# Performance work log

Measured on AMD Instinct MI355X. Metric: run time of the kernel, lower is better.

Reference implementation:

```python
import jax, jax.numpy as jnp
import numpy as np

B, T, D = 16, 512, 256          # batch, seq_len, d_model (= num features = num graph nodes N)
H, MC, K, DE, DH = 4, 4, 3, 10, 128
GS, SS, AS = 4, 6, 4            # global/sector/asset regime states
TAU = 0.5
STEPS = 3                       # diffusion steps
HID = max(64, D)
DEC_H = max(64, D // 2)


def setup_inputs() -> dict:
    key = jax.random.key(0)
    ks = iter(jax.random.split(key, 64))

    def nrm(shape, s=0.02):
        return (s * jax.random.normal(next(ks), shape)).astype(jnp.float32)

    z = lambda *s: jnp.zeros(s, jnp.float32)
    o = lambda *s: jnp.ones(s, jnp.float32)
    p = dict(
        x=jax.random.normal(next(ks), (B, T, D), dtype=jnp.float32),
        # hierarchical regime controller
        gW1=nrm((D, HID)), gb1=z(HID), g_ln_w=o(HID), g_ln_b=z(HID),
        gW2=nrm((HID, GS)), gb2=z(GS),
        sW1=nrm((D, HID)), sb1=z(HID), sW2=nrm((HID, D * SS)), sb2=z(D * SS),
        aW1=nrm((D, HID)), ab1=z(HID), aW2=nrm((HID, D * AS)), ab2=z(D * AS),
        global_prior=z(GS), sector_prior=z(SS), asset_prior=z(AS),
        g2f=nrm((GS, D)),
        sector_emb=jax.random.normal(next(ks), (SS, D), dtype=jnp.float32),
        asset_emb=jax.random.normal(next(ks), (AS, D), dtype=jnp.float32),
        # bidirectional temporal scan (BI-Mamba stand-in)
        decay_f=nrm((D,), 1.0), decay_b=nrm((D,), 1.0),
        tW=nrm((D, D)), tb=z(D),
        # Bayesian MAGAC + diffusion graph prior
        psi=nrm((H, D, DE), 0.1), log_sigma=jnp.full((H,), -2.0, jnp.float32),
        step_logits=jnp.linspace(-1.0, 0.5, STEPS).astype(jnp.float32),
        noise_scale=jnp.full((STEPS,), 0.05, jnp.float32),
        Wk=nrm((K + 1, T, DH)),
        mean_w=nrm((DH,)), mean_b=z(), lv_w=nrm((DH,)), lv_b=z(),
        # risk-aware decoder
        dW1=nrm((D, DEC_H)), db1=z(DEC_H), d_ln_w=o(DEC_H), d_ln_b=z(DEC_H),
        mW=nrm((DEC_H,)), mb=z(), lvW=nrm((DEC_H,)), lvb=z(),
        cW=nrm((DEC_H,)), cb=z(),
    )
    return p


def _ln(h, w, b):
    m = h.mean(-1, keepdims=True)
    v = h.var(-1, keepdims=True)  # biased, matches torch LayerNorm
    return (h - m) / jnp.sqrt(v + 1e-5) * w + b


def _gelu(h):
    return jax.nn.gelu(h, approximate=False)


def _gumbel_softmax(k, logits):
    u = jax.random.uniform(k, logits.shape, minval=1e-6, maxval=1.0 - 1e-6)
    g = -jnp.log(-jnp.log(u))
    return jax.nn.softmax((logits + g) / TAU, axis=-1)


def _fwd(x, gW1, gb1, g_ln_w, g_ln_b, gW2, gb2, sW1, sb1, sW2, sb2,
         aW1, ab1, aW2, ab2, global_prior, sector_prior, asset_prior,
         g2f, sector_emb, asset_emb, decay_f, decay_b, tW, tb,
         psi, log_sigma, step_logits, noise_scale, Wk,
         mean_w, mean_b, lv_w, lv_b,
         dW1, db1, d_ln_w, d_ln_b, mW, mb, lvW, lvb, cW, cb):
    rk = jax.random.key(42)
    k_g, k_s, k_a, k_eps, k_diff = jax.random.split(rk, 5)

    # ---- hierarchical regime controller ----
    seq_mean = x.mean(1)                               # (B, D)
    diff_summary = (x[:, 1:] - x[:, :-1]).mean(1)      # (B, D)
    g_logits = _gelu(_ln(seq_mean @ gW1 + gb1, g_ln_w, g_ln_b)) @ gW2 + gb2
    s_logits = (_gelu(seq_mean @ sW1 + sb1) @ sW2 + sb2).reshape(B, D, SS)
    a_logits = (_gelu(diff_summary @ aW1 + ab1) @ aW2 + ab2).reshape(B, D, AS)
    g_probs = _gumbel_softmax(k_g, g_logits)
    s_probs = _gumbel_softmax(k_s, s_logits)
    a_probs = _gumbel_softmax(k_a, a_logits)
    global_gate = g_probs @ g2f                                   # (B, D)
    # diagonal of einsum('bfs,sd->bfd') == einsum('bfs,sf->bf')
    sector_gate = jnp.einsum('bfs,sf->bf', s_probs, sector_emb)
    asset_gate = jnp.einsum('bfs,sf->bf', a_probs, asset_emb)
    feature_gate = jax.nn.sigmoid(global_gate + sector_gate + asset_gate)
    gated_x = x * feature_gate[:, None, :]

    # ---- bidirectional temporal EMA scan (BI-Mamba stand-in) ----
    af = jax.nn.sigmoid(decay_f)
    abk = jax.nn.sigmoid(decay_b)
    xs = gated_x.transpose(1, 0, 2)                    # (T, B, D)

    def ema(a):
        def step(h, xt):
            h = a * h + (1.0 - a) * xt
            return h, h
        return step

    _, hf = jax.lax.scan(ema(af), jnp.zeros_like(xs[0]), xs)
    _, hb = jax.lax.scan(ema(abk), jnp.zeros_like(xs[0]), xs[::-1])
    temporal = (hf + hb[::-1]).transpose(1, 0, 2) @ tW + tb       # (B, T, D)
    node_major = temporal.transpose(0, 2, 1)                      # (B, N=D, T)

    # ---- Bayesian adjacency sampling (MC samples per head) ----
    logits = jnp.einsum('hne,hme->hnm', psi, psi) / jnp.sqrt(jnp.float32(DE))
    sigma = jnp.exp(log_sigma)                                    # (H,)
    eps = jax.random.normal(k_eps, (MC, H, D, D))
    A = jax.nn.softmax(logits[None] + sigma[None, :, None, None] * eps, axis=-1)

    # ---- diffusion refinement guided by regime features ----
    ctx = feature_gate.mean(0)
    ctx = ctx / (jnp.linalg.norm(ctx) + 1e-6)
    outer = ctx[:, None] * ctx[None, :]
    outer = outer / jnp.maximum(outer.sum(-1, keepdims=True), 1e-6)
    dkeys = jax.random.split(k_diff, STEPS)
    for s in range(STEPS):                             # fixed small loop, vectorized over (MC,H)
        alpha = jax.nn.sigmoid(step_logits[s])
        noise = noise_scale[s] * jax.random.normal(dkeys[s], A.shape)
        A = alpha * A + (1.0 - alpha) * outer + noise
        A = 0.5 * (A + jnp.swapaxes(A, -1, -2))
        A = jax.nn.softmax(A, axis=-1)

    # ---- K-hop graph conv, averaged over MC samples and heads ----
    Z = jnp.einsum('bnt,td->bnd', node_major, Wk[0])[None, None]  # hop 0
    P = jnp.broadcast_to(node_major, (MC, H, B, D, T))
    for k in range(1, K + 1):
        P = jnp.einsum('mhnp,mhbpt->mhbnt', A, P)
        Z = Z + jnp.einsum('mhbnt,td->mhbnd', P, Wk[k])
    Z = Z.mean((0, 1))                                            # (B, N, DH)
    graph_mean = Z @ mean_w + mean_b                              # (B, N)
    graph_logvar = Z @ lv_w + lv_b                                # (B, N)

    # ---- risk-aware decoder ----
    feat = _ln(_gelu(graph_mean @ dW1 + db1), d_ln_w, d_ln_b)     # (B, DEC_H)
    mean = feat @ mW + mb
    dec_logvar = feat @ lvW + lvb
    _cvar = jax.nn.sigmoid(feat @ cW + cb)  # auxiliary head (not in returned output)
    var = jnp.exp(dec_logvar) + jnp.exp(graph_logvar).sum(1)
    log_var = jnp.log(var)
    return jnp.stack([mean, log_var], axis=-1)                    # (B, 2)


def reference(x, gW1, gb1, g_ln_w, g_ln_b, gW2, gb2, sW1, sb1, sW2, sb2,
              aW1, ab1, aW2, ab2, global_prior, sector_prior, asset_prior,
              g2f, sector_emb, asset_emb, decay_f, decay_b, tW, tb,
              psi, log_sigma, step_logits, noise_scale, Wk,
              mean_w, mean_b, lv_w, lv_b,
              dW1, db1, d_ln_w, d_ln_b, mW, mb, lvW, lvb, cW, cb):
    return _fwd(x, gW1, gb1, g_ln_w, g_ln_b, gW2, gb2, sW1, sb1, sW2, sb2,
                aW1, ab1, aW2, ab2, global_prior, sector_prior, asset_prior,
                g2f, sector_emb, asset_emb, decay_f, decay_b, tW, tb,
                psi, log_sigma, step_logits, noise_scale, Wk,
                mean_w, mean_b, lv_w, lv_b,
                dW1, db1, d_ln_w, d_ln_b, mW, mb, lvW, lvb, cW, cb)
```

## Files before the change

### kernel.cpp

```cpp
#include <hip/hip_runtime.h>
#include <stdint.h>

#define PARTITIONABLE 1

namespace {

struct TFPair { uint32_t a, b; };

__host__ __device__ constexpr uint32_t rotl32(uint32_t x, int d) {
  return (x << d) | (x >> (32 - d));
}

__host__ __device__ constexpr TFPair tf2x32(uint32_t k0, uint32_t k1,
                                            uint32_t x0, uint32_t x1) {
  uint32_t k2 = k0 ^ k1 ^ 0x1BD11BDAu;
  x0 += k0; x1 += k1;
  x0 += x1; x1 = rotl32(x1, 13); x1 ^= x0;
  x0 += x1; x1 = rotl32(x1, 15); x1 ^= x0;
  x0 += x1; x1 = rotl32(x1, 26); x1 ^= x0;
  x0 += x1; x1 = rotl32(x1, 6);  x1 ^= x0;
  x0 += k1; x1 += k2 + 1u;
  x0 += x1; x1 = rotl32(x1, 17); x1 ^= x0;
  x0 += x1; x1 = rotl32(x1, 29); x1 ^= x0;
  x0 += x1; x1 = rotl32(x1, 16); x1 ^= x0;
  x0 += x1; x1 = rotl32(x1, 24); x1 ^= x0;
  x0 += k2; x1 += k0 + 2u;
  x0 += x1; x1 = rotl32(x1, 13); x1 ^= x0;
  x0 += x1; x1 = rotl32(x1, 15); x1 ^= x0;
  x0 += x1; x1 = rotl32(x1, 26); x1 ^= x0;
  x0 += x1; x1 = rotl32(x1, 6);  x1 ^= x0;
  x0 += k0; x1 += k1 + 3u;
  x0 += x1; x1 = rotl32(x1, 17); x1 ^= x0;
  x0 += x1; x1 = rotl32(x1, 29); x1 ^= x0;
  x0 += x1; x1 = rotl32(x1, 16); x1 ^= x0;
  x0 += x1; x1 = rotl32(x1, 24); x1 ^= x0;
  x0 += k1; x1 += k2 + 4u;
  x0 += x1; x1 = rotl32(x1, 13); x1 ^= x0;
  x0 += x1; x1 = rotl32(x1, 15); x1 ^= x0;
  x0 += x1; x1 = rotl32(x1, 26); x1 ^= x0;
  x0 += x1; x1 = rotl32(x1, 6);  x1 ^= x0;
  x0 += k2; x1 += k0 + 5u;
  return TFPair{x0, x1};
}

#if PARTITIONABLE
constexpr TFPair KG  = tf2x32(0u, 42u, 0u, 0u);
constexpr TFPair KS  = tf2x32(0u, 42u, 0u, 1u);
constexpr TFPair KA  = tf2x32(0u, 42u, 0u, 2u);
constexpr TFPair KE  = tf2x32(0u, 42u, 0u, 3u);
constexpr TFPair KD  = tf2x32(0u, 42u, 0u, 4u);
constexpr TFPair DK0 = tf2x32(KD.a, KD.b, 0u, 0u);
constexpr TFPair DK1 = tf2x32(KD.a, KD.b, 0u, 1u);
constexpr TFPair DK2 = tf2x32(KD.a, KD.b, 0u, 2u);
#else
constexpr TFPair SP0 = tf2x32(0u, 42u, 0u, 5u);
constexpr TFPair SP1 = tf2x32(0u, 42u, 1u, 6u);
constexpr TFPair SP2 = tf2x32(0u, 42u, 2u, 7u);
constexpr TFPair SP3 = tf2x32(0u, 42u, 3u, 8u);
constexpr TFPair SP4 = tf2x32(0u, 42u, 4u, 9u);
constexpr TFPair KG  = TFPair{SP0.a, SP1.a};
constexpr TFPair KS  = TFPair{SP2.a, SP3.a};
constexpr TFPair KA  = TFPair{SP4.a, SP0.b};
constexpr TFPair KE  = TFPair{SP1.b, SP2.b};
constexpr TFPair KD  = TFPair{SP3.b, SP4.b};
constexpr TFPair DP0 = tf2x32(KD.a, KD.b, 0u, 3u);
constexpr TFPair DP1 = tf2x32(KD.a, KD.b, 1u, 4u);
constexpr TFPair DP2 = tf2x32(KD.a, KD.b, 2u, 5u);
constexpr TFPair DK0 = TFPair{DP0.a, DP1.a};
constexpr TFPair DK1 = TFPair{DP2.a, DP0.b};
constexpr TFPair DK2 = TFPair{DP1.b, DP2.b};
#endif

__device__ __forceinline__ uint32_t rbits(uint32_t k0, uint32_t k1,
                                          uint32_t idx, uint32_t half) {
#if PARTITIONABLE
  TFPair t = tf2x32(k0, k1, 0u, idx);
  return t.a ^ t.b;
#else
  if (idx < half) return tf2x32(k0, k1, idx, idx + half).a;
  return tf2x32(k0, k1, idx - half, idx).b;
#endif
}

__device__ __forceinline__ float bits_to_u01(uint32_t bits) {
  return __uint_as_float((bits >> 9) | 0x3F800000u) - 1.0f;
}

__device__ __forceinline__ float gumbel_u(uint32_t k0, uint32_t k1,
                                          uint32_t idx, uint32_t half) {
  const float mn = 1e-6f;
  const float mx = 1.0f - 1e-6f;
  float f = bits_to_u01(rbits(k0, k1, idx, half));
  return fmaxf(mn, f * (mx - mn) + mn);
}

__device__ __forceinline__ float erfinv_f32(float x) {
  float w = -log1pf(-x * x);
  float p;
  if (w < 5.0f) {
    w -= 2.5f;
    p = 2.81022636e-08f;
    p = fmaf(p, w, 3.43273939e-07f);
    p = fmaf(p, w, -3.5233877e-06f);
    p = fmaf(p, w, -4.39150654e-06f);
    p = fmaf(p, w, 0.00021858087f);
    p = fmaf(p, w, -0.00125372503f);
    p = fmaf(p, w, -0.00417768164f);
    p = fmaf(p, w, 0.246640727f);
    p = fmaf(p, w, 1.50140941f);
  } else {
    w = sqrtf(w) - 3.0f;
    p = -0.000200214257f;
    p = fmaf(p, w, 0.000100950558f);
    p = fmaf(p, w, 0.00134934322f);
    p = fmaf(p, w, -0.00367342844f);
    p = fmaf(p, w, 0.00573950773f);
    p = fmaf(p, w, -0.0076224613f);
    p = fmaf(p, w, 0.00943887047f);
    p = fmaf(p, w, 1.00167406f);
    p = fmaf(p, w, 2.83297682f);
  }
  return p * x;
}

__device__ __forceinline__ float normal_from(uint32_t k0, uint32_t k1,
                                             uint32_t idx, uint32_t half) {
  const float lo = -0x1.fffffep-1f;
  float f = bits_to_u01(rbits(k0, k1, idx, half));
  float u = fmaxf(lo, f * 2.0f + lo);
  return 1.41421356237f * erfinv_f32(u);
}

__device__ __forceinline__ float gelu_f(float x) {
  return 0.5f * x * (1.0f + erff(x / 1.4142135623730951f));
}
__device__ __forceinline__ float sigmoid_f(float x) {
  return 1.0f / (1.0f + expf(-x));
}

__device__ __forceinline__ float wave_sum(float v) {
  #pragma unroll
  for (int m = 32; m > 0; m >>= 1) v += __shfl_xor(v, m);
  return v;
}
__device__ __forceinline__ float wave_max(float v) {
  #pragma unroll
  for (int m = 32; m > 0; m >>= 1) v = fmaxf(v, __shfl_xor(v, m));
  return v;
}
template <int NW>
__device__ __forceinline__ float blk_sum(float v, float* slots) {
  v = wave_sum(v);
  int wid = threadIdx.x >> 6;
  if ((threadIdx.x & 63) == 0) slots[wid] = v;
  __syncthreads();
  float r = slots[0];
  #pragma unroll
  for (int i = 1; i < NW; ++i) r += slots[i];
  return r;
}
template <int NW>
__device__ __forceinline__ float blk_max(float v, float* slots) {
  v = wave_max(v);
  int wid = threadIdx.x >> 6;
  if ((threadIdx.x & 63) == 0) slots[wid] = v;
  __syncthreads();
  float r = slots[0];
  #pragma unroll
  for (int i = 1; i < NW; ++i) r = fmaxf(r, slots[i]);
  return r;
}

struct Params {
  const float *x, *gW1, *gb1, *glnw, *glnb, *gW2, *gb2, *sW1, *sb1, *sW2, *sb2,
      *aW1, *ab1, *aW2, *ab2, *g2f, *semb, *aemb, *decay_f, *decay_b, *tW, *tb,
      *psi, *log_sigma, *step_logits, *noise_scale, *Wk, *mean_w, *mean_b,
      *lv_w, *lv_b, *dW1, *db1, *dlnw, *dlnb, *mW, *mb, *lvW, *lvb;
  float* out;
  float *ps, *ds, *hgG, *hgS, *hgA, *fg, *ctx, *v, *sv, *u, *Pf, *Qf, *Pb, *Qb,
      *Lf, *Lb, *YH, *R1, *R2, *gm, *glv, *A, *A2;
};


__device__ __forceinline__ void phase_hidden(const Params& P, float* smem,
                                             int bid, int tid) {
  float* inv = smem;
  float* s1 = smem + 256;
  float* s2 = smem + 260;
  int head = bid >> 4, b = bid & 15;
  float iv;
  if (head < 2) {
    float s = 0.f;
    for (int tc = 0; tc < 16; ++tc) s += P.ps[(size_t)(b * 16 + tc) * 256 + tid];
    iv = s / 512.0f;
  } else {
    iv = P.ds[b * 256 + tid];
  }
  inv[tid] = iv;
  __syncthreads();
  const float* W1 = (head == 0) ? P.gW1 : (head == 1) ? P.sW1 : P.aW1;
  const float* b1 = (head == 0) ? P.gb1 : (head == 1) ? P.sb1 : P.ab1;
  float h = b1[tid];
  for (int d = 0; d < 256; ++d) h = fmaf(inv[d], W1[d * 256 + tid], h);
  if (head == 0) {
    float mean = blk_sum<4>(h, s1) / 256.0f;
    float dv = h - mean;
    float var = blk_sum<4>(dv * dv, s2) / 256.0f;
    h = dv / sqrtf(var + 1e-5f) * P.glnw[tid] + P.glnb[tid];
  }
  float* outp = (head == 0) ? P.hgG : (head == 1) ? P.hgS : P.hgA;
  outp[b * 256 + tid] = gelu_f(h);
}

__device__ __forceinline__ void phase_vcompute(const Params& P, int bid2,
                                               int tid) {
  int j = bid2 >> 2, tg = bid2 & 3;
  const float* wp = (j & 1) ? P.lv_w : P.mean_w;
  const float* Wkk = P.Wk + (size_t)(j >> 1) * 65536;
  int wid = tid >> 6, lane = tid & 63;
  float w0 = wp[lane], w1 = wp[64 + lane];
  float svloc = 0.f;
  for (int i = 0; i < 32; ++i) {
    int t = tg * 128 + wid * 32 + i;
    const float* row = Wkk + (size_t)t * 128;
    float s = row[lane] * w0 + row[64 + lane] * w1;
    s = wave_sum(s);
    if (lane == 0) { P.v[j * 512 + t] = s; svloc += s; }
  }
  if (lane == 0) atomicAdd(&P.sv[j], svloc);
}

__device__ __forceinline__ void phase_ainit_row(const Params& P, float* smem,
                                                int blk, int tid) {
  float* pn = smem;
  float* s1 = smem + 12;
  float* s2 = smem + 16;
  int mh = blk >> 8, h = mh & 3, n = blk & 255, p = tid;
  if (p < 10) pn[p] = P.psi[(size_t)(h * 256 + n) * 10 + p];
  __syncthreads();
  const float* pp = P.psi + (size_t)(h * 256 + p) * 10;
  float s = 0.f;
  #pragma unroll
  for (int e = 0; e < 10; ++e) s = fmaf(pn[e], pp[e], s);
  float logit = s / sqrtf(10.0f);
  uint32_t idx = (uint32_t)blk * 256u + (uint32_t)p;
  float eps = normal_from(KE.a, KE.b, idx, 524288u);
  float val = logit + expf(P.log_sigma[h]) * eps;
  float mx = blk_max<4>(val, s1);
  float e = expf(val - mx);
  float sum = blk_sum<4>(e, s2);
  P.A[(size_t)blk * 256 + p] = e / sum;
}

__device__ __forceinline__ void phase_gates(const Params& P, float* smem,
                                            int bid, int tid) {
  float* hgGs = smem;
  float* hgSs = smem + 256;
  float* hgAs = smem + 512;
  float* lvS = smem + 768;
  float* lvA = smem + 1152;
  float* gsl = smem + 1408;
  float* gvals = smem + 1424;
  float* gpv = smem + 1428;
  int b = bid >> 2, f0 = (bid & 3) * 64;
  hgGs[tid] = P.hgG[b * 256 + tid];
  hgSs[tid] = P.hgS[b * 256 + tid];
  hgAs[tid] = P.hgA[b * 256 + tid];
  __syncthreads();
  float lg[4];
  #pragma unroll
  for (int s = 0; s < 4; ++s)
    lg[s] = blk_sum<4>(hgGs[tid] * P.gW2[tid * 4 + s], gsl + 4 * s);
  if (tid < 4) {
    float u = gumbel_u(KG.a, KG.b, (uint32_t)(b * 4 + tid), 32u);
    float g = -logf(-logf(u));
    gvals[tid] = (lg[tid] + P.gb2[tid] + g) / 0.5f;
  }
  __syncthreads();
  if (tid < 4) {
    float mx = fmaxf(fmaxf(gvals[0], gvals[1]), fmaxf(gvals[2], gvals[3]));
    float sum = expf(gvals[0] - mx) + expf(gvals[1] - mx) +
                expf(gvals[2] - mx) + expf(gvals[3] - mx);
    gpv[tid] = expf(gvals[tid] - mx) / sum;
  }
  {
    int o = tid;
    int fl = o / 6, s = o - fl * 6;
    int f = f0 + fl;
    const float* wp = P.sW2 + f * 6 + s;
    float acc = P.sb2[f * 6 + s];
    for (int d = 0; d < 256; ++d) acc = fmaf(hgSs[d], wp[(size_t)d * 1536], acc);
    float u = gumbel_u(KS.a, KS.b, (uint32_t)(b * 256 + f) * 6u + s, 12288u);
    lvS[o] = (acc + (-logf(-logf(u)))) / 0.5f;
  }
  if (tid < 128) {
    int o = tid + 256;
    int fl = o / 6, s = o - fl * 6;
    int f = f0 + fl;
    const float* wp = P.sW2 + f * 6 + s;
    float acc = P.sb2[f * 6 + s];
    for (int d = 0; d < 256; ++d) acc = fmaf(hgSs[d], wp[(size_t)d * 1536], acc);
    float u = gumbel_u(KS.a, KS.b, (uint32_t)(b * 256 + f) * 6u + s, 12288u);
    lvS[o] = (acc + (-logf(-logf(u)))) / 0.5f;
  }
  {
    int fl = tid >> 2, s = tid & 3;
    int f = f0 + fl;
    const float* wp = P.aW2 + f * 4 + s;
    float acc = P.ab2[f * 4 + s];
    for (int d = 0; d < 256; ++d) acc = fmaf(hgAs[d], wp[(size_t)d * 1024], acc);
    float u = gumbel_u(KA.a, KA.b, (uint32_t)(b * 256 + f) * 4u + s, 8192u);
    lvA[tid] = (acc + (-logf(-logf(u)))) / 0.5f;
  }
  __syncthreads();
  if (tid < 64) {
    int f = f0 + tid;
    float v0 = lvS[tid * 6 + 0], v1 = lvS[tid * 6 + 1], v2 = lvS[tid * 6 + 2];
    float v3 = lvS[tid * 6 + 3], v4 = lvS[tid * 6 + 4], v5 = lvS[tid * 6 + 5];
    float mx = fmaxf(fmaxf(fmaxf(v0, v1), fmaxf(v2, v3)), fmaxf(v4, v5));
    float e0 = expf(v0 - mx), e1 = expf(v1 - mx), e2 = expf(v2 - mx);
    float e3 = expf(v3 - mx), e4 = expf(v4 - mx), e5 = expf(v5 - mx);
    float ssum = e0 + e1 + e2 + e3 + e4 + e5;
    float sg = (e0 / ssum) * P.semb[0 * 256 + f] + (e1 / ssum) * P.semb[1 * 256 + f] +
               (e2 / ssum) * P.semb[2 * 256 + f] + (e3 / ssum) * P.semb[3 * 256 + f] +
               (e4 / ssum) * P.semb[4 * 256 + f] + (e5 / ssum) * P.semb[5 * 256 + f];
    float a0 = lvA[tid * 4 + 0], a1 = lvA[tid * 4 + 1];
    float a2 = lvA[tid * 4 + 2], a3 = lvA[tid * 4 + 3];
    float amx = fmaxf(fmaxf(a0, a1), fmaxf(a2, a3));
    float x0 = expf(a0 - amx), x1 = expf(a1 - amx);
    float x2 = expf(a2 - amx), x3 = expf(a3 - amx);
    float asum = x0 + x1 + x2 + x3;
    float ag = (x0 / asum) * P.aemb[0 * 256 + f] + (x1 / asum) * P.aemb[1 * 256 + f] +
               (x2 / asum) * P.aemb[2 * 256 + f] + (x3 / asum) * P.aemb[3 * 256 + f];
    float gg = 0.f;
    #pragma unroll
    for (int s = 0; s < 4; ++s) gg = fmaf(gpv[s], P.g2f[s * 256 + f], gg);
    P.fg[b * 256 + f] = sigmoid_f(gg + sg + ag);
  }
}

__device__ __forceinline__ void phase_ctx(const Params& P, float* smem,
                                          int tid) {
  float* s1 = smem;
  float* s2 = smem + 4;
  float c = 0.f;
  for (int b = 0; b < 16; ++b) c += P.fg[b * 256 + tid];
  c /= 16.0f;
  float ss = blk_sum<4>(c * c, s1);
  float cv = c / (sqrtf(ss) + 1e-6f);
  P.ctx[tid] = cv;
  float S = blk_sum<4>(cv, s2);
  if (tid == 0) P.ctx[256] = S;
}

__device__ __forceinline__ void phase_scan1(const Params& P, float* smem,
                                            int ch, int tid) {
  float* vv = smem;
  int b = ch >> 4, c = ch & 15;
  int d = tid;
  vv[(d >> 5) * 32 + (d & 31)] = P.v[(d >> 5) * 512 + c * 32 + (d & 31)];
  __syncthreads();
  float g = P.fg[b * 256 + d];
  float af = sigmoid_f(P.decay_f[d]);
  float ab = sigmoid_f(P.decay_b[d]);
  float r_gx[32];
  const float* xp = P.x + ((size_t)b * 512 + c * 32) * 256 + d;
  #pragma unroll
  for (int i = 0; i < 32; ++i) r_gx[i] = xp[(size_t)i * 256] * g;
  float h = 0.f, pw = 1.f;
  float Pr[8], Q[8];
  #pragma unroll
  for (int j = 0; j < 8; ++j) { Pr[j] = 0.f; Q[j] = 0.f; }
  #pragma unroll
  for (int i = 0; i < 32; ++i) {
    h = fmaf(af, h, (1.0f - af) * r_gx[i]);
    pw *= af;
    #pragma unroll
    for (int j = 0; j < 8; ++j) {
      float vj = vv[j * 32 + i];
      Pr[j] = fmaf(h, vj, Pr[j]);
      Q[j] = fmaf(pw, vj, Q[j]);
    }
  }
  size_t base = ((size_t)(b * 16 + c) * 8) * 256 + d;
  #pragma unroll
  for (int j = 0; j < 8; ++j) {
    P.Pf[base + j * 256] = Pr[j];
    P.Qf[base + j * 256] = Q[j];
  }
  P.Lf[(b * 16 + c) * 256 + d] = h;
  h = 0.f; pw = 1.f;
  #pragma unroll
  for (int j = 0; j < 8; ++j) { Pr[j] = 0.f; Q[j] = 0.f; }
  #pragma unroll
  for (int i = 31; i >= 0; --i) {
    h = fmaf(ab, h, (1.0f - ab) * r_gx[i]);
    pw *= ab;
    #pragma unroll
    for (int j = 0; j < 8; ++j) {
      float vj = vv[j * 32 + i];
      Pr[j] = fmaf(h, vj, Pr[j]);
      Q[j] = fmaf(pw, vj, Q[j]);
    }
  }
  #pragma unroll
  for (int j = 0; j < 8; ++j) {
    P.Pb[base + j * 256] = Pr[j];
    P.Qb[base + j * 256] = Q[j];
  }
  P.Lb[(b * 16 + c) * 256 + d] = h;
}

__device__ __forceinline__ void phase_scan2(const Params& P, int blk, int tid) {
  int b = blk >> 3, j = blk & 7;
  int d = tid;
  float af = sigmoid_f(P.decay_f[d]);
  float ab = sigmoid_f(P.decay_b[d]);
  float af32 = af, ab32 = ab;
  #pragma unroll
  for (int q = 0; q < 5; ++q) { af32 *= af32; ab32 *= ab32; }
  float acc = 0.f, H = 0.f;
  for (int c = 0; c < 16; ++c) {
    size_t base = ((size_t)(b * 16 + c) * 8 + j) * 256 + d;
    acc += P.Pf[base] + H * P.Qf[base];
    H = P.Lf[(b * 16 + c) * 256 + d] + af32 * H;
  }
  H = 0.f;
  for (int c = 15; c >= 0; --c) {
    size_t base = ((size_t)(b * 16 + c) * 8 + j) * 256 + d;
    acc += P.Pb[base] + H * P.Qb[base];
    H = P.Lb[(b * 16 + c) * 256 + d] + ab32 * H;
  }
  P.u[(b * 8 + j) * 256 + d] = acc;
}

__device__ __forceinline__ void phase_ygemm(const Params& P, float* smem,
                                            int blk32, int tid) {
  float* As = smem;
  float* Bs = smem + 1056;
  float* svs = smem + 2112;
  int n0 = (blk32 & 7) * 32, m0 = (blk32 >> 3) * 32;
  int tx = tid & 31, ty = tid >> 5;
  if (tid < 8) svs[tid] = P.sv[tid];
  float acc[4] = {0.f, 0.f, 0.f, 0.f};
  for (int k0 = 0; k0 < 256; k0 += 32) {
    #pragma unroll
    for (int l = 0; l < 4; ++l) {
      int e = tid + l * 256, r = e >> 5, cc = e & 31;
      As[r * 33 + cc] = P.u[(size_t)(m0 + r) * 256 + k0 + cc];
      Bs[r * 33 + cc] = P.tW[(size_t)(k0 + r) * 256 + n0 + cc];
    }
    __syncthreads();
    #pragma unroll
    for (int kk = 0; kk < 32; ++kk) {
      float bv = Bs[kk * 33 + tx];
      #pragma unroll
      for (int i = 0; i < 4; ++i)
        acc[i] = fmaf(As[(ty + 8 * i) * 33 + kk], bv, acc[i]);
    }
    __syncthreads();
  }
  int n = n0 + tx;
  float tbn = P.tb[n];
  float mb0 = P.mean_b[0], lb0 = P.lv_b[0];
  #pragma unroll
  for (int i = 0; i < 4; ++i) {
    int row = m0 + ty + 8 * i;
    int b = row >> 3, j = row & 7;
    float val = acc[i] + tbn * svs[j];
    if (j == 0) P.gm[b * 256 + n] = val + mb0;
    else if (j == 1) P.glv[b * 256 + n] = val + lb0;
    else {
      int k = (j >> 1) - 1, proj = j & 1;
      P.YH[k * 8192 + n * 32 + b * 2 + proj] = val;
    }
  }
}

__device__ __forceinline__ void phase_mix_row(const Params& P, float* smem,
                                              int sidx, const float* Ain,
                                              float* Aout, uint32_t dk0,
                                              uint32_t dk1, int blk, int tid) {
  float* s1 = smem;
  float* s2 = smem + 4;
  float alpha = sigmoid_f(P.step_logits[sidx]);
  float ns = P.noise_scale[sidx];
  float S = P.ctx[256];
  float cp = P.ctx[tid];
  int mh = blk >> 8, n = blk & 255, p = tid;
  float cn = P.ctx[n];
  float o_np = (cn * cp) / fmaxf(cn * S, 1e-6f);
  float o_pn = (cp * cn) / fmaxf(cp * S, 1e-6f);
  uint32_t i_np = (uint32_t)blk * 256u + (uint32_t)p;
  uint32_t i_pn = (uint32_t)mh * 65536u + (uint32_t)p * 256u + (uint32_t)n;
  float a_np = Ain[(size_t)mh * 65536 + n * 256 + p];
  float a_pn = Ain[(size_t)mh * 65536 + p * 256 + n];
  float m_np = alpha * a_np + (1.0f - alpha) * o_np +
               ns * normal_from(dk0, dk1, i_np, 524288u);
  float m_pn = alpha * a_pn + (1.0f - alpha) * o_pn +
               ns * normal_from(dk0, dk1, i_pn, 524288u);
  float val = 0.5f * (m_np + m_pn);
  float mx = blk_max<4>(val, s1);
  float e = expf(val - mx);
  float sum = blk_sum<4>(e, s2);
  Aout[(size_t)blk * 256 + p] = e / sum;
}

__device__ __forceinline__ void phase_horner(const Params& P, float* smem,
                                             const float* A, const float* Rin,
                                             int sRin, const float* Yadd,
                                             float* Rout, int bid, int tid) {
  float* As = smem;
  float* Bs = smem + 1056;
  int nt = bid & 7, mh = bid >> 3;
  int n0 = nt * 32;
  int tx = tid & 31, ty = tid >> 5;
  float acc[4] = {0.f, 0.f, 0.f, 0.f};
  const float* Ab = A + (size_t)mh * 65536;
  const float* Rb = Rin + (size_t)mh * sRin;
  for (int k0 = 0; k0 < 256; k0 += 32) {
    #pragma unroll
    for (int l = 0; l < 4; ++l) {
      int e = tid + l * 256, r = e >> 5, cc = e & 31;
      As[r * 33 + cc] = Ab[(size_t)(n0 + r) * 256 + k0 + cc];
      Bs[r * 33 + cc] = Rb[(size_t)(k0 + r) * 32 + cc];
    }
    __syncthreads();
    #pragma unroll
    for (int kk = 0; kk < 32; ++kk) {
      float bv = Bs[kk * 33 + tx];
      #pragma unroll
      for (int i = 0; i < 4; ++i)
        acc[i] = fmaf(As[(ty + 8 * i) * 33 + kk], bv, acc[i]);
    }
    __syncthreads();
  }
  #pragma unroll
  for (int i = 0; i < 4; ++i) {
    int n = n0 + ty + 8 * i;
    float vv = acc[i];
    if (Yadd) vv += Yadd[n * 32 + tx];
    Rout[(size_t)mh * 8192 + (size_t)n * 32 + tx] = vv;
  }
}

__device__ __forceinline__ void phase_findec(const Params& P, float* smem,
                                             int bid, int tid) {
  float* gmv = smem;
  float* sl = smem + 256;
  int b = bid;
  float sm_ = 0.f, sl_ = 0.f;
  for (int mh = 0; mh < 16; ++mh) {
    sm_ += P.R1[(size_t)mh * 8192 + tid * 32 + b * 2];
    sl_ += P.R1[(size_t)mh * 8192 + tid * 32 + b * 2 + 1];
  }
  float gmn = P.gm[b * 256 + tid] + sm_ * (1.0f / 16.0f);
  float gln = P.glv[b * 256 + tid] + sl_ * (1.0f / 16.0f);
  gmv[tid] = gmn;
  float se = expf(gln);
  __syncthreads();
  float sumexp = blk_sum<4>(se, sl);
  float h = 0.f;
  if (tid < 128) {
    h = P.db1[tid];
    for (int n = 0; n < 256; ++n) h = fmaf(gmv[n], P.dW1[n * 128 + tid], h);
    h = gelu_f(h);
  }
  float mean = blk_sum<4>(tid < 128 ? h : 0.f, sl + 4) / 128.0f;
  float dv = (tid < 128) ? h - mean : 0.f;
  float var = blk_sum<4>(dv * dv, sl + 8) / 128.0f;
  float feat = (tid < 128) ? dv / sqrtf(var + 1e-5f) * P.dlnw[tid] + P.dlnb[tid]
                           : 0.f;
  float m_c = blk_sum<4>(tid < 128 ? feat * P.mW[tid] : 0.f, sl + 12) + P.mb[0];
  float lv_c = blk_sum<4>(tid < 128 ? feat * P.lvW[tid] : 0.f, sl + 16) + P.lvb[0];
  if (tid == 0) {
    P.out[b * 2 + 0] = m_c;
    P.out[b * 2 + 1] = logf(expf(lv_c) + sumexp);
  }
}


__global__ __launch_bounds__(256) void kL0(Params P) {
  int bid = blockIdx.x, tid = threadIdx.x;
  int b = bid >> 4, tc = bid & 15;
  const float* xp = P.x + ((size_t)b * 512 + tc * 32) * 256 + tid;
  float s = 0.f;
  for (int i = 0; i < 32; ++i) s += xp[(size_t)i * 256];
  P.ps[(size_t)bid * 256 + tid] = s;
  if (tc == 0) {
    const float* xb = P.x + (size_t)b * 512 * 256 + tid;
    P.ds[b * 256 + tid] = (xb[(size_t)511 * 256] - xb[0]) / 511.0f;
  }
  if (bid == 0 && tid < 8) P.sv[tid] = 0.f;
}

__global__ __launch_bounds__(256) void kLA(Params P) {
  __shared__ float smem[20];
  phase_ainit_row(P, smem, blockIdx.x, threadIdx.x);
}

__global__ __launch_bounds__(256) void kLB(Params P) {
  __shared__ float smem[272];
  int bid = blockIdx.x, tid = threadIdx.x;
  if (bid < 48) phase_hidden(P, smem, bid, tid);
  else phase_vcompute(P, bid - 48, tid);
}

__global__ __launch_bounds__(256) void kLC(Params P) {
  __shared__ float smem[1440];
  phase_gates(P, smem, blockIdx.x, threadIdx.x);
}

__global__ __launch_bounds__(256) void kLD(Params P) {
  __shared__ float smem[256];
  int bid = blockIdx.x, tid = threadIdx.x;
  if (bid < 256) phase_scan1(P, smem, bid, tid);
  else phase_ctx(P, smem, tid);
}

__global__ __launch_bounds__(256) void kM0(Params P) {
  __shared__ float smem[8];
  int bid = blockIdx.x, tid = threadIdx.x;
  if (bid < 4096) phase_mix_row(P, smem, 0, P.A, P.A2, DK0.a, DK0.b, bid, tid);
  else phase_scan2(P, bid - 4096, tid);
}

__global__ __launch_bounds__(256) void kM1(Params P) {
  __shared__ float smem[2120];
  int bid = blockIdx.x, tid = threadIdx.x;
  if (bid < 4096) phase_mix_row(P, smem, 1, P.A2, P.A, DK1.a, DK1.b, bid, tid);
  else phase_ygemm(P, smem, bid - 4096, tid);
}

__global__ __launch_bounds__(256) void kM2(Params P) {
  __shared__ float smem[8];
  phase_mix_row(P, smem, 2, P.A, P.A2, DK2.a, DK2.b, blockIdx.x, threadIdx.x);
}

__global__ __launch_bounds__(256) void kH1(Params P) {
  __shared__ float smem[2112];
  phase_horner(P, smem, P.A2, P.YH + 2 * 8192, 0, P.YH + 8192, P.R1,
               blockIdx.x, threadIdx.x);
}
__global__ __launch_bounds__(256) void kH2(Params P) {
  __shared__ float smem[2112];
  phase_horner(P, smem, P.A2, P.R1, 8192, P.YH, P.R2, blockIdx.x, threadIdx.x);
}
__global__ __launch_bounds__(256) void kH3(Params P) {
  __shared__ float smem[2112];
  phase_horner(P, smem, P.A2, P.R2, 8192, nullptr, P.R1, blockIdx.x,
               threadIdx.x);
}

__global__ __launch_bounds__(256) void kFin(Params P) {
  __shared__ float smem[276];
  phase_findec(P, smem, blockIdx.x, threadIdx.x);
}

constexpr size_t O_PS = 0;
constexpr size_t O_DS = 65536;
constexpr size_t O_HGG = 69632;
constexpr size_t O_HGS = 73728;
constexpr size_t O_HGA = 77824;
constexpr size_t O_FG = 81920;
constexpr size_t O_CTX = 86016;
constexpr size_t O_V = 86336;
constexpr size_t O_SV = 90432;
constexpr size_t O_U = 90496;
constexpr size_t O_PF = 123264;
constexpr size_t O_QF = 647552;
constexpr size_t O_PB = 1171840;
constexpr size_t O_QB = 1696128;
constexpr size_t O_LF = 2220416;
constexpr size_t O_LB = 2285952;
constexpr size_t O_YH = 2351488;
constexpr size_t O_R1 = 2376064;
constexpr size_t O_R2 = 2507136;
constexpr size_t O_GM = 2638208;
constexpr size_t O_GLV = 2642304;
constexpr size_t O_A = 2646400;
constexpr size_t O_A2 = 3694976;

}

extern "C" void kernel_launch(void* const* d_in, const int* in_sizes, int n_in,
                              void* d_out, int out_size, void* d_ws,
                              size_t ws_size, hipStream_t stream) {
  (void)in_sizes; (void)n_in; (void)out_size; (void)ws_size;
  float* w = (float*)d_ws;
  Params prm;
  prm.x = (const float*)d_in[0];
  prm.gW1 = (const float*)d_in[1];
  prm.gb1 = (const float*)d_in[2];
  prm.glnw = (const float*)d_in[3];
  prm.glnb = (const float*)d_in[4];
  prm.gW2 = (const float*)d_in[5];
  prm.gb2 = (const float*)d_in[6];
  prm.sW1 = (const float*)d_in[7];
  prm.sb1 = (const float*)d_in[8];
  prm.sW2 = (const float*)d_in[9];
  prm.sb2 = (const float*)d_in[10];
  prm.aW1 = (const float*)d_in[11];
  prm.ab1 = (const float*)d_in[12];
  prm.aW2 = (const float*)d_in[13];
  prm.ab2 = (const float*)d_in[14];
  prm.g2f = (const float*)d_in[18];
  prm.semb = (const float*)d_in[19];
  prm.aemb = (const float*)d_in[20];
  prm.decay_f = (const float*)d_in[21];
  prm.decay_b = (const float*)d_in[22];
  prm.tW = (const float*)d_in[23];
  prm.tb = (const float*)d_in[24];
  prm.psi = (const float*)d_in[25];
  prm.log_sigma = (const float*)d_in[26];
  prm.step_logits = (const float*)d_in[27];
  prm.noise_scale = (const float*)d_in[28];
  prm.Wk = (const float*)d_in[29];
  prm.mean_w = (const float*)d_in[30];
  prm.mean_b = (const float*)d_in[31];
  prm.lv_w = (const float*)d_in[32];
  prm.lv_b = (const float*)d_in[33];
  prm.dW1 = (const float*)d_in[34];
  prm.db1 = (const float*)d_in[35];
  prm.dlnw = (const float*)d_in[36];
  prm.dlnb = (const float*)d_in[37];
  prm.mW = (const float*)d_in[38];
  prm.mb = (const float*)d_in[39];
  prm.lvW = (const float*)d_in[40];
  prm.lvb = (const float*)d_in[41];
  prm.out = (float*)d_out;
  prm.ps = w + O_PS;
  prm.ds = w + O_DS;
  prm.hgG = w + O_HGG;
  prm.hgS = w + O_HGS;
  prm.hgA = w + O_HGA;
  prm.fg = w + O_FG;
  prm.ctx = w + O_CTX;
  prm.v = w + O_V;
  prm.sv = w + O_SV;
  prm.u = w + O_U;
  prm.Pf = w + O_PF;
  prm.Qf = w + O_QF;
  prm.Pb = w + O_PB;
  prm.Qb = w + O_QB;
  prm.Lf = w + O_LF;
  prm.Lb = w + O_LB;
  prm.YH = w + O_YH;
  prm.R1 = w + O_R1;
  prm.R2 = w + O_R2;
  prm.gm = w + O_GM;
  prm.glv = w + O_GLV;
  prm.A = w + O_A;
  prm.A2 = w + O_A2;

  kL0<<<256, 256, 0, stream>>>(prm);
  kLA<<<4096, 256, 0, stream>>>(prm);
  kLB<<<80, 256, 0, stream>>>(prm);
  kLC<<<64, 256, 0, stream>>>(prm);
  kLD<<<257, 256, 0, stream>>>(prm);
  kM0<<<4224, 256, 0, stream>>>(prm);
  kM1<<<4128, 256, 0, stream>>>(prm);
  kM2<<<4096, 256, 0, stream>>>(prm);
  kH1<<<128, 256, 0, stream>>>(prm);
  kH2<<<128, 256, 0, stream>>>(prm);
  kH3<<<128, 256, 0, stream>>>(prm);
  kFin<<<16, 256, 0, stream>>>(prm);
}
```

Before: 311.2 us.

## Merge twelve kernel launches into one cooperative persistent kernel with grid syncs

Replaces the chain of twelve separate kernel launches with a single cooperative kernel that loops over work items in each phase and separates phases with grid.sync. It also fuses the sequence-mean and hidden-layer computation into the gate phase per block, which drops the ps/ds/hg workspace buffers, and replaces the atomicAdd accumulation of sv with per-wave partial slots that are summed later. The aim is to remove launch gaps and intermediate global traffic. In exchange, the hidden MLP is now recomputed redundantly in each of the four feature-group blocks per batch. Grid-wide barriers, a grid capped at 768 blocks, and a launch bound of 3 blocks per CU may also limit parallelism in the large phases.

```diff
diff --git a/kernel.cpp b/kernel.cpp
--- a/kernel.cpp
+++ b/kernel.cpp
@@ -1,7 +1,10 @@
 #include <hip/hip_runtime.h>
+#include <hip/hip_cooperative_groups.h>
 #include <stdint.h>
 
 #define PARTITIONABLE 1
+
+namespace cg = cooperative_groups;
 
 namespace {
 
@@ -177,100 +180,57 @@
       *psi, *log_sigma, *step_logits, *noise_scale, *Wk, *mean_w, *mean_b,
       *lv_w, *lv_b, *dW1, *db1, *dlnw, *dlnb, *mW, *mb, *lvW, *lvb;
   float* out;
-  float *ps, *ds, *hgG, *hgS, *hgA, *fg, *ctx, *v, *sv, *u, *Pf, *Qf, *Pb, *Qb,
-      *Lf, *Lb, *YH, *R1, *R2, *gm, *glv, *A, *A2;
+  float *fg, *ctx, *v, *sv, *u, *Pf, *Qf, *Pb, *Qb, *Lf, *Lb, *YH, *R1, *R2,
+      *gm, *glv, *A, *A2;
 };
 
 
-__device__ __forceinline__ void phase_hidden(const Params& P, float* smem,
-                                             int bid, int tid) {
-  float* inv = smem;
-  float* s1 = smem + 256;
-  float* s2 = smem + 260;
-  int head = bid >> 4, b = bid & 15;
-  float iv;
-  if (head < 2) {
-    float s = 0.f;
-    for (int tc = 0; tc < 16; ++tc) s += P.ps[(size_t)(b * 16 + tc) * 256 + tid];
-    iv = s / 512.0f;
-  } else {
-    iv = P.ds[b * 256 + tid];
-  }
-  inv[tid] = iv;
-  __syncthreads();
-  const float* W1 = (head == 0) ? P.gW1 : (head == 1) ? P.sW1 : P.aW1;
-  const float* b1 = (head == 0) ? P.gb1 : (head == 1) ? P.sb1 : P.ab1;
-  float h = b1[tid];
-  for (int d = 0; d < 256; ++d) h = fmaf(inv[d], W1[d * 256 + tid], h);
-  if (head == 0) {
-    float mean = blk_sum<4>(h, s1) / 256.0f;
-    float dv = h - mean;
+__device__ __forceinline__ void phase_hidgates(const Params& P, float* smem,
+                                               int task, int tid) {
+  float* seqm = smem;
+  float* dif  = smem + 256;
+  float* hgGs = smem + 512;
+  float* hgSs = smem + 768;
+  float* hgAs = smem + 1024;
+  float* lvS  = smem + 1280;
+  float* lvA  = smem + 1664;
+  float* gsl  = smem + 1920;
+  float* gvals= smem + 1936;
+  float* gpv  = smem + 1940;
+  float* s1   = smem + 1944;
+  float* s2   = smem + 1948;
+  int b = task >> 2, f0 = (task & 3) * 64;
+  const float* xb = P.x + (size_t)b * 512 * 256 + tid;
+  float s = 0.f;
+  for (int tc = 0; tc < 16; ++tc) {
+    float ps = 0.f;
+    for (int i = 0; i < 32; ++i) ps += xb[(size_t)(tc * 32 + i) * 256];
+    s += ps;
+  }
+  seqm[tid] = s / 512.0f;
+  dif[tid] = (xb[(size_t)511 * 256] - xb[0]) / 511.0f;
+  __syncthreads();
+  float hG = P.gb1[tid], hS = P.sb1[tid], hA = P.ab1[tid];
+  for (int d = 0; d < 256; ++d) {
+    float sm = seqm[d], df = dif[d];
+    hG = fmaf(sm, P.gW1[d * 256 + tid], hG);
+    hS = fmaf(sm, P.sW1[d * 256 + tid], hS);
+    hA = fmaf(df, P.aW1[d * 256 + tid], hA);
+  }
+  {
+    float mean = blk_sum<4>(hG, s1) / 256.0f;
+    float dv = hG - mean;
     float var = blk_sum<4>(dv * dv, s2) / 256.0f;
-    h = dv / sqrtf(var + 1e-5f) * P.glnw[tid] + P.glnb[tid];
-  }
-  float* outp = (head == 0) ? P.hgG : (head == 1) ? P.hgS : P.hgA;
-  outp[b * 256 + tid] = gelu_f(h);
-}
-
-__device__ __forceinline__ void phase_vcompute(const Params& P, int bid2,
-                                               int tid) {
-  int j = bid2 >> 2, tg = bid2 & 3;
-  const float* wp = (j & 1) ? P.lv_w : P.mean_w;
-  const float* Wkk = P.Wk + (size_t)(j >> 1) * 65536;
-  int wid = tid >> 6, lane = tid & 63;
-  float w0 = wp[lane], w1 = wp[64 + lane];
-  float svloc = 0.f;
-  for (int i = 0; i < 32; ++i) {
-    int t = tg * 128 + wid * 32 + i;
-    const float* row = Wkk + (size_t)t * 128;
-    float s = row[lane] * w0 + row[64 + lane] * w1;
-    s = wave_sum(s);
-    if (lane == 0) { P.v[j * 512 + t] = s; svloc += s; }
-  }
-  if (lane == 0) atomicAdd(&P.sv[j], svloc);
-}
-
-__device__ __forceinline__ void phase_ainit_row(const Params& P, float* smem,
-                                                int blk, int tid) {
-  float* pn = smem;
-  float* s1 = smem + 12;
-  float* s2 = smem + 16;
-  int mh = blk >> 8, h = mh & 3, n = blk & 255, p = tid;
-  if (p < 10) pn[p] = P.psi[(size_t)(h * 256 + n) * 10 + p];
-  __syncthreads();
-  const float* pp = P.psi + (size_t)(h * 256 + p) * 10;
-  float s = 0.f;
-  #pragma unroll
-  for (int e = 0; e < 10; ++e) s = fmaf(pn[e], pp[e], s);
-  float logit = s / sqrtf(10.0f);
-  uint32_t idx = (uint32_t)blk * 256u + (uint32_t)p;
-  float eps = normal_from(KE.a, KE.b, idx, 524288u);
-  float val = logit + expf(P.log_sigma[h]) * eps;
-  float mx = blk_max<4>(val, s1);
-  float e = expf(val - mx);
-  float sum = blk_sum<4>(e, s2);
-  P.A[(size_t)blk * 256 + p] = e / sum;
-}
-
-__device__ __forceinline__ void phase_gates(const Params& P, float* smem,
-                                            int bid, int tid) {
-  float* hgGs = smem;
-  float* hgSs = smem + 256;
-  float* hgAs = smem + 512;
-  float* lvS = smem + 768;
-  float* lvA = smem + 1152;
-  float* gsl = smem + 1408;
-  float* gvals = smem + 1424;
-  float* gpv = smem + 1428;
-  int b = bid >> 2, f0 = (bid & 3) * 64;
-  hgGs[tid] = P.hgG[b * 256 + tid];
-  hgSs[tid] = P.hgS[b * 256 + tid];
-  hgAs[tid] = P.hgA[b * 256 + tid];
+    hG = dv / sqrtf(var + 1e-5f) * P.glnw[tid] + P.glnb[tid];
+  }
+  hgGs[tid] = gelu_f(hG);
+  hgSs[tid] = gelu_f(hS);
+  hgAs[tid] = gelu_f(hA);
   __syncthreads();
   float lg[4];
   #pragma unroll
-  for (int s = 0; s < 4; ++s)
-    lg[s] = blk_sum<4>(hgGs[tid] * P.gW2[tid * 4 + s], gsl + 4 * s);
+  for (int sx = 0; sx < 4; ++sx)
+    lg[sx] = blk_sum<4>(hgGs[tid] * P.gW2[tid * 4 + sx], gsl + 4 * sx);
   if (tid < 4) {
     float u = gumbel_u(KG.a, KG.b, (uint32_t)(b * 4 + tid), 32u);
     float g = -logf(-logf(u));
@@ -285,31 +245,31 @@
   }
   {
     int o = tid;
-    int fl = o / 6, s = o - fl * 6;
+    int fl = o / 6, sx = o - fl * 6;
     int f = f0 + fl;
-    const float* wp = P.sW2 + f * 6 + s;
-    float acc = P.sb2[f * 6 + s];
+    const float* wp = P.sW2 + f * 6 + sx;
+    float acc = P.sb2[f * 6 + sx];
     for (int d = 0; d < 256; ++d) acc = fmaf(hgSs[d], wp[(size_t)d * 1536], acc);
-    float u = gumbel_u(KS.a, KS.b, (uint32_t)(b * 256 + f) * 6u + s, 12288u);
+    float u = gumbel_u(KS.a, KS.b, (uint32_t)(b * 256 + f) * 6u + sx, 12288u);
     lvS[o] = (acc + (-logf(-logf(u)))) / 0.5f;
   }
   if (tid < 128) {
     int o = tid + 256;
-    int fl = o / 6, s = o - fl * 6;
+    int fl = o / 6, sx = o - fl * 6;
     int f = f0 + fl;
-    const float* wp = P.sW2 + f * 6 + s;
-    float acc = P.sb2[f * 6 + s];
+    const float* wp = P.sW2 + f * 6 + sx;
+    float acc = P.sb2[f * 6 + sx];
     for (int d = 0; d < 256; ++d) acc = fmaf(hgSs[d], wp[(size_t)d * 1536], acc);
-    float u = gumbel_u(KS.a, KS.b, (uint32_t)(b * 256 + f) * 6u + s, 12288u);
+    float u = gumbel_u(KS.a, KS.b, (uint32_t)(b * 256 + f) * 6u + sx, 12288u);
     lvS[o] = (acc + (-logf(-logf(u)))) / 0.5f;
   }
   {
-    int fl = tid >> 2, s = tid & 3;
+    int fl = tid >> 2, sx = tid & 3;
     int f = f0 + fl;
-    const float* wp = P.aW2 + f * 4 + s;
-    float acc = P.ab2[f * 4 + s];
+    const float* wp = P.aW2 + f * 4 + sx;
+    float acc = P.ab2[f * 4 + sx];
     for (int d = 0; d < 256; ++d) acc = fmaf(hgAs[d], wp[(size_t)d * 1024], acc);
-    float u = gumbel_u(KA.a, KA.b, (uint32_t)(b * 256 + f) * 4u + s, 8192u);
+    float u = gumbel_u(KA.a, KA.b, (uint32_t)(b * 256 + f) * 4u + sx, 8192u);
     lvA[tid] = (acc + (-logf(-logf(u)))) / 0.5f;
   }
   __syncthreads();
@@ -334,9 +294,49 @@
                (x2 / asum) * P.aemb[2 * 256 + f] + (x3 / asum) * P.aemb[3 * 256 + f];
     float gg = 0.f;
     #pragma unroll
-    for (int s = 0; s < 4; ++s) gg = fmaf(gpv[s], P.g2f[s * 256 + f], gg);
+    for (int sx = 0; sx < 4; ++sx) gg = fmaf(gpv[sx], P.g2f[sx * 256 + f], gg);
     P.fg[b * 256 + f] = sigmoid_f(gg + sg + ag);
   }
+}
+
+__device__ __forceinline__ void phase_vcompute(const Params& P, int bid2,
+                                               int tid) {
+  int j = bid2 >> 2, tg = bid2 & 3;
+  const float* wp = (j & 1) ? P.lv_w : P.mean_w;
+  const float* Wkk = P.Wk + (size_t)(j >> 1) * 65536;
+  int wid = tid >> 6, lane = tid & 63;
+  float w0 = wp[lane], w1 = wp[64 + lane];
+  float svloc = 0.f;
+  for (int i = 0; i < 32; ++i) {
+    int t = tg * 128 + wid * 32 + i;
+    const float* row = Wkk + (size_t)t * 128;
+    float s = row[lane] * w0 + row[64 + lane] * w1;
+    s = wave_sum(s);
+    if (lane == 0) { P.v[j * 512 + t] = s; svloc += s; }
+  }
+  if (lane == 0) P.sv[j * 16 + tg * 4 + wid] = svloc;
+}
+
+__device__ __forceinline__ void phase_ainit_row(const Params& P, float* smem,
+                                                int blk, int tid) {
+  float* pn = smem;
+  float* s1 = smem + 12;
+  float* s2 = smem + 16;
+  int mh = blk >> 8, h = mh & 3, n = blk & 255, p = tid;
+  if (p < 10) pn[p] = P.psi[(size_t)(h * 256 + n) * 10 + p];
+  __syncthreads();
+  const float* pp = P.psi + (size_t)(h * 256 + p) * 10;
+  float s = 0.f;
+  #pragma unroll
+  for (int e = 0; e < 10; ++e) s = fmaf(pn[e], pp[e], s);
+  float logit = s / sqrtf(10.0f);
+  uint32_t idx = (uint32_t)blk * 256u + (uint32_t)p;
+  float eps = normal_from(KE.a, KE.b, idx, 524288u);
+  float val = logit + expf(P.log_sigma[h]) * eps;
+  float mx = blk_max<4>(val, s1);
+  float e = expf(val - mx);
+  float sum = blk_sum<4>(e, s2);
+  P.A[(size_t)blk * 256 + p] = e / sum;
 }
 
 __device__ __forceinline__ void phase_ctx(const Params& P, float* smem,
@@ -441,7 +441,12 @@
   float* svs = smem + 2112;
   int n0 = (blk32 & 7) * 32, m0 = (blk32 >> 3) * 32;
   int tx = tid & 31, ty = tid >> 5;
-  if (tid < 8) svs[tid] = P.sv[tid];
+  if (tid < 8) {
+    float ssv = 0.f;
+    #pragma unroll
+    for (int q = 0; q < 16; ++q) ssv += P.sv[tid * 16 + q];
+    svs[tid] = ssv;
+  }
   float acc[4] = {0.f, 0.f, 0.f, 0.f};
   for (int k0 = 0; k0 < 256; k0 += 32) {
     #pragma unroll
@@ -580,106 +585,97 @@
 }
 
 
-__global__ __launch_bounds__(256) void kL0(Params P) {
-  int bid = blockIdx.x, tid = threadIdx.x;
-  int b = bid >> 4, tc = bid & 15;
-  const float* xp = P.x + ((size_t)b * 512 + tc * 32) * 256 + tid;
-  float s = 0.f;
-  for (int i = 0; i < 32; ++i) s += xp[(size_t)i * 256];
-  P.ps[(size_t)bid * 256 + tid] = s;
-  if (tc == 0) {
-    const float* xb = P.x + (size_t)b * 512 * 256 + tid;
-    P.ds[b * 256 + tid] = (xb[(size_t)511 * 256] - xb[0]) / 511.0f;
-  }
-  if (bid == 0 && tid < 8) P.sv[tid] = 0.f;
-}
-
-__global__ __launch_bounds__(256) void kLA(Params P) {
-  __shared__ float smem[20];
-  phase_ainit_row(P, smem, blockIdx.x, threadIdx.x);
-}
-
-__global__ __launch_bounds__(256) void kLB(Params P) {
-  __shared__ float smem[272];
-  int bid = blockIdx.x, tid = threadIdx.x;
-  if (bid < 48) phase_hidden(P, smem, bid, tid);
-  else phase_vcompute(P, bid - 48, tid);
-}
-
-__global__ __launch_bounds__(256) void kLC(Params P) {
-  __shared__ float smem[1440];
-  phase_gates(P, smem, blockIdx.x, threadIdx.x);
-}
-
-__global__ __launch_bounds__(256) void kLD(Params P) {
-  __shared__ float smem[256];
-  int bid = blockIdx.x, tid = threadIdx.x;
-  if (bid < 256) phase_scan1(P, smem, bid, tid);
-  else phase_ctx(P, smem, tid);
-}
-
-__global__ __launch_bounds__(256) void kM0(Params P) {
-  __shared__ float smem[8];
-  int bid = blockIdx.x, tid = threadIdx.x;
-  if (bid < 4096) phase_mix_row(P, smem, 0, P.A, P.A2, DK0.a, DK0.b, bid, tid);
-  else phase_scan2(P, bid - 4096, tid);
-}
-
-__global__ __launch_bounds__(256) void kM1(Params P) {
-  __shared__ float smem[2120];
-  int bid = blockIdx.x, tid = threadIdx.x;
-  if (bid < 4096) phase_mix_row(P, smem, 1, P.A2, P.A, DK1.a, DK1.b, bid, tid);
-  else phase_ygemm(P, smem, bid - 4096, tid);
-}
-
-__global__ __launch_bounds__(256) void kM2(Params P) {
-  __shared__ float smem[8];
-  phase_mix_row(P, smem, 2, P.A, P.A2, DK2.a, DK2.b, blockIdx.x, threadIdx.x);
-}
-
-__global__ __launch_bounds__(256) void kH1(Params P) {
-  __shared__ float smem[2112];
-  phase_horner(P, smem, P.A2, P.YH + 2 * 8192, 0, P.YH + 8192, P.R1,
-               blockIdx.x, threadIdx.x);
-}
-__global__ __launch_bounds__(256) void kH2(Params P) {
-  __shared__ float smem[2112];
-  phase_horner(P, smem, P.A2, P.R1, 8192, P.YH, P.R2, blockIdx.x, threadIdx.x);
-}
-__global__ __launch_bounds__(256) void kH3(Params P) {
-  __shared__ float smem[2112];
-  phase_horner(P, smem, P.A2, P.R2, 8192, nullptr, P.R1, blockIdx.x,
-               threadIdx.x);
-}
-
-__global__ __launch_bounds__(256) void kFin(Params P) {
-  __shared__ float smem[276];
-  phase_findec(P, smem, blockIdx.x, threadIdx.x);
-}
-
-constexpr size_t O_PS = 0;
-constexpr size_t O_DS = 65536;
-constexpr size_t O_HGG = 69632;
-constexpr size_t O_HGS = 73728;
-constexpr size_t O_HGA = 77824;
-constexpr size_t O_FG = 81920;
-constexpr size_t O_CTX = 86016;
-constexpr size_t O_V = 86336;
-constexpr size_t O_SV = 90432;
-constexpr size_t O_U = 90496;
-constexpr size_t O_PF = 123264;
-constexpr size_t O_QF = 647552;
-constexpr size_t O_PB = 1171840;
-constexpr size_t O_QB = 1696128;
-constexpr size_t O_LF = 2220416;
-constexpr size_t O_LB = 2285952;
-constexpr size_t O_YH = 2351488;
-constexpr size_t O_R1 = 2376064;
-constexpr size_t O_R2 = 2507136;
-constexpr size_t O_GM = 2638208;
-constexpr size_t O_GLV = 2642304;
-constexpr size_t O_A = 2646400;
-constexpr size_t O_A2 = 3694976;
+__global__ __launch_bounds__(256, 3) void kMega(Params P) {
+  __shared__ float smem[2176];
+  cg::grid_group grid = cg::this_grid();
+  const int tid = threadIdx.x;
+  const int nb = gridDim.x;
+
+  for (int t = blockIdx.x; t < 4192; t += nb) {
+    __syncthreads();
+    if (t < 64) phase_hidgates(P, smem, t, tid);
+    else if (t < 96) phase_vcompute(P, t - 64, tid);
+    else phase_ainit_row(P, smem, t - 96, tid);
+  }
+  __threadfence();
+  grid.sync();
+
+  for (int t = blockIdx.x; t < 257; t += nb) {
+    __syncthreads();
+    if (t < 256) phase_scan1(P, smem, t, tid);
+    else phase_ctx(P, smem, tid);
+  }
+  __threadfence();
+  grid.sync();
+
+  for (int t = blockIdx.x; t < 4224; t += nb) {
+    __syncthreads();
+    if (t < 4096) phase_mix_row(P, smem, 0, P.A, P.A2, DK0.a, DK0.b, t, tid);
+    else phase_scan2(P, t - 4096, tid);
+  }
+  __threadfence();
+  grid.sync();
+
+  for (int t = blockIdx.x; t < 4128; t += nb) {
+    __syncthreads();
+    if (t < 4096) phase_mix_row(P, smem, 1, P.A2, P.A, DK1.a, DK1.b, t, tid);
+    else phase_ygemm(P, smem, t - 4096, tid);
+  }
+  __threadfence();
+  grid.sync();
+
+  for (int t = blockIdx.x; t < 4096; t += nb) {
+    __syncthreads();
+    phase_mix_row(P, smem, 2, P.A, P.A2, DK2.a, DK2.b, t, tid);
+  }
+  __threadfence();
+  grid.sync();
+
+  for (int t = blockIdx.x; t < 128; t += nb) {
+    __syncthreads();
+    phase_horner(P, smem, P.A2, P.YH + 2 * 8192, 0, P.YH + 8192, P.R1, t, tid);
+  }
+  __threadfence();
+  grid.sync();
+
+  for (int t = blockIdx.x; t < 128; t += nb) {
+    __syncthreads();
+    phase_horner(P, smem, P.A2, P.R1, 8192, P.YH, P.R2, t, tid);
+  }
+  __threadfence();
+  grid.sync();
+
+  for (int t = blockIdx.x; t < 128; t += nb) {
+    __syncthreads();
+    phase_horner(P, smem, P.A2, P.R2, 8192, nullptr, P.R1, t, tid);
+  }
+  __threadfence();
+  grid.sync();
+
+  for (int t = blockIdx.x; t < 16; t += nb) {
+    __syncthreads();
+    phase_findec(P, smem, t, tid);
+  }
+}
+
+constexpr size_t O_FG = 0;
+constexpr size_t O_CTX = 4096;
+constexpr size_t O_V = 4480;
+constexpr size_t O_SV = 8576;
+constexpr size_t O_U = 8704;
+constexpr size_t O_PF = 41472;
+constexpr size_t O_QF = 565760;
+constexpr size_t O_PB = 1090048;
+constexpr size_t O_QB = 1614336;
+constexpr size_t O_LF = 2138624;
+constexpr size_t O_LB = 2204160;
+constexpr size_t O_YH = 2269696;
+constexpr size_t O_R1 = 2294272;
+constexpr size_t O_R2 = 2425344;
+constexpr size_t O_GM = 2556416;
+constexpr size_t O_GLV = 2560512;
+constexpr size_t O_A = 2564608;
+constexpr size_t O_A2 = 3613184;
 
 }
 
@@ -729,11 +725,6 @@
   prm.lvW = (const float*)d_in[40];
   prm.lvb = (const float*)d_in[41];
   prm.out = (float*)d_out;
-  prm.ps = w + O_PS;
-  prm.ds = w + O_DS;
-  prm.hgG = w + O_HGG;
-  prm.hgS = w + O_HGS;
-  prm.hgA = w + O_HGA;
   prm.fg = w + O_FG;
   prm.ctx = w + O_CTX;
   prm.v = w + O_V;
@@ -753,16 +744,17 @@
   prm.A = w + O_A;
   prm.A2 = w + O_A2;
 
-  kL0<<<256, 256, 0, stream>>>(prm);
-  kLA<<<4096, 256, 0, stream>>>(prm);
-  kLB<<<80, 256, 0, stream>>>(prm);
-  kLC<<<64, 256, 0, stream>>>(prm);
-  kLD<<<257, 256, 0, stream>>>(prm);
-  kM0<<<4224, 256, 0, stream>>>(prm);
-  kM1<<<4128, 256, 0, stream>>>(prm);
-  kM2<<<4096, 256, 0, stream>>>(prm);
-  kH1<<<128, 256, 0, stream>>>(prm);
-  kH2<<<128, 256, 0, stream>>>(prm);
-  kH3<<<128, 256, 0, stream>>>(prm);
-  kFin<<<16, 256, 0, stream>>>(prm);
-}
+  static int nblk = 0;
+  if (nblk == 0) {
+    int maxb = 0;
+    if (hipOccupancyMaxActiveBlocksPerMultiprocessor(&maxb, kMega, 256, 0) !=
+            hipSuccess ||
+        maxb < 1)
+      maxb = 1;
+    nblk = maxb * 256;
+    if (nblk > 768) nblk = 768;
+  }
+
+  void* args[] = {(void*)&prm};
+  hipLaunchCooperativeKernel(kMega, dim3(nblk), dim3(256), args, 0, stream);
+}
```

New measurement: 919.7 us. 196% more time.
